# Kernel optimization log

Measured on AMD Instinct MI355X. Metric: run time of the kernel, lower is better.

## Reference

```python
import jax, jax.numpy as jnp
import numpy as np
from functools import partial

B, N, K = 64, 1001, 10  # batch, n_nodes (incl. depot), n_clusters


def setup_inputs() -> dict:
    key = jax.random.key(0)
    k1, k2, k3 = jax.random.split(key, 3)
    cluster_logits = jax.random.normal(k1, (B, N, K), dtype=jnp.float32)
    coords = jax.random.uniform(k2, (B, N, 2), dtype=jnp.float32)
    demands = jax.random.uniform(k3, (B, N), dtype=jnp.float32)
    capacity = jnp.ones((B,), dtype=jnp.float32) * 5.0
    return {"cluster_logits": cluster_logits, "coords": coords,
            "demands": demands, "capacity": capacity, "n_samples": 1}


def _routing_distance(depot, cust, dem, cap, assign, n_clusters):
    """Total NN-heuristic routing distance for one instance.
    depot: (2,), cust: (n,2), dem: (n,), cap: scalar, assign: (n,) int.
    """
    n = cust.shape[0]
    S = n_clusters * n  # max routes: route id = cluster * n + within-cluster route idx

    # --- greedy capacity split (sequential over customers in index order) ---
    def split_step(carry, x):
        loads, counts, nonempty = carry  # per-cluster state
        k, d = x
        start_new = (loads[k] + d > cap) & nonempty[k]
        new_count = counts[k] + start_new.astype(jnp.int32)
        new_load = jnp.where(start_new, d, loads[k] + d)
        carry = (loads.at[k].set(new_load), counts.at[k].set(new_count),
                 nonempty.at[k].set(True))
        return carry, new_count

    init = (jnp.zeros((n_clusters,), dem.dtype),
            jnp.zeros((n_clusters,), jnp.int32),
            jnp.zeros((n_clusters,), bool))
    _, rid = jax.lax.scan(split_step, init, (assign.astype(jnp.int32), dem))
    seg = assign.astype(jnp.int32) * n + rid  # global route id per customer

    # --- nearest-neighbor routing, all routes advance one hop per scan step ---
    idx = jnp.arange(n)

    def nn_step(carry, _):
        visited, pos, acc = carry  # (n,), (S,2), (S,)
        cur = pos[seg]  # (n,2) current position of each customer's route
        d = jnp.sqrt(((cust - cur) ** 2).sum(-1))
        d = jnp.where(visited, jnp.inf, d)
        seg_min = jax.ops.segment_min(d, seg, num_segments=S)  # (S,)
        win = (~visited) & (d <= seg_min[seg])
        # lowest-index tie-break, matching the torch strict-< argmin
        win_idx = jax.ops.segment_min(jnp.where(win, idx, n), seg, num_segments=S)
        active = win_idx < n
        chosen = win & (idx == win_idx[seg])
        visited = visited | chosen
        acc = acc + jnp.where(active, seg_min, 0.0)
        new_pos = jnp.where(active[:, None], cust[jnp.clip(win_idx, 0, n - 1)], pos)
        return (visited, new_pos, acc), None

    pos0 = jnp.broadcast_to(depot, (S, 2))
    carry0 = (jnp.zeros((n,), bool), pos0, jnp.zeros((S,), cust.dtype))
    (visited, pos, acc), _ = jax.lax.scan(nn_step, carry0, None, length=n)

    # return-to-depot leg for every non-empty route
    route_used = jax.ops.segment_sum(jnp.ones((n,), cust.dtype), seg, num_segments=S) > 0
    acc = acc + jnp.where(route_used, jnp.sqrt(((pos - depot) ** 2).sum(-1)), 0.0)
    return acc.sum()


def _route_batch(coords, demands, capacity, assign, n_clusters):
    f = partial(_routing_distance, n_clusters=n_clusters)
    return jax.vmap(f)(coords[:, 0], coords[:, 1:], demands[:, 1:], capacity, assign)


def reference(cluster_logits, coords, demands, capacity, n_samples):
    batch_size, n_nodes, n_clusters = cluster_logits.shape
    customer_logits = cluster_logits[:, 1:, :]  # drop depot
    log_probs = jax.nn.log_softmax(customer_logits, axis=-1)

    key = jax.random.key(42)
    all_d, all_lp = [], []
    for s in range(n_samples):  # tiny fixed loop over samples
        ks = jax.random.fold_in(key, s)
        assignments = jax.random.categorical(ks, customer_logits, axis=-1)  # (B, n)
        slp = jnp.take_along_axis(log_probs, assignments[..., None], axis=-1)[..., 0]
        all_lp.append(slp.sum(-1))  # (B,)
        d = jax.lax.stop_gradient(
            _route_batch(coords, demands, capacity, assignments, n_clusters))
        all_d.append(d)

    distances = jnp.stack(all_d, axis=1)       # (B, n_samples)
    log_probs_stacked = jnp.stack(all_lp, axis=1)
    if n_samples > 1:
        baseline = jax.lax.stop_gradient(distances.mean(axis=1, keepdims=True))
    else:
        baseline = jax.lax.stop_gradient(distances.mean())
    advantage = distances - baseline
    reinforce_loss = (advantage * log_probs_stacked).sum() / (batch_size * n_samples)
    return reinforce_loss, distances.mean()
```

## Files before the change

### kernel.cpp

```cpp
#include <hip/hip_runtime.h>
#include <stdint.h>

#define BB 64
#define NC 1000
#define KC 10
#define MEMCAP 212
#define RCAP 64

__host__ __device__ inline void threefry2x32(uint32_t k0, uint32_t k1,
                                             uint32_t x0, uint32_t x1,
                                             uint32_t* o0, uint32_t* o1) {
  uint32_t k2 = k0 ^ k1 ^ 0x1BD11BDAu;
  x0 += k0; x1 += k1;
#define TF_R(R) { x0 += x1; x1 = (x1 << (R)) | (x1 >> (32 - (R))); x1 ^= x0; }
  TF_R(13) TF_R(15) TF_R(26) TF_R(6)
  x0 += k1; x1 += k2 + 1u;
  TF_R(17) TF_R(29) TF_R(16) TF_R(24)
  x0 += k2; x1 += k0 + 2u;
  TF_R(13) TF_R(15) TF_R(26) TF_R(6)
  x0 += k0; x1 += k1 + 3u;
  TF_R(17) TF_R(29) TF_R(16) TF_R(24)
  x0 += k1; x1 += k2 + 4u;
  TF_R(13) TF_R(15) TF_R(26) TF_R(6)
  x0 += k2; x1 += k0 + 5u;
#undef TF_R
  *o0 = x0; *o1 = x1;
}

__device__ inline uint32_t rand_bits(uint32_t ks0, uint32_t ks1, uint32_t p) {
  uint32_t a, b; threefry2x32(ks0, ks1, 0u, p, &a, &b); return b;
}

template <int CTRL>
__device__ __forceinline__ void dpp_min_step(unsigned long long& comb,
                                             float& x, float& y) {
  int lo = (int)(uint32_t)comb;
  int hi = (int)(uint32_t)(comb >> 32);
  int olo = __builtin_amdgcn_update_dpp(lo, lo, CTRL, 0xf, 0xf, false);
  int ohi = __builtin_amdgcn_update_dpp(hi, hi, CTRL, 0xf, 0xf, false);
  int oxi = __builtin_amdgcn_update_dpp(__float_as_int(x), __float_as_int(x),
                                        CTRL, 0xf, 0xf, false);
  int oyi = __builtin_amdgcn_update_dpp(__float_as_int(y), __float_as_int(y),
                                        CTRL, 0xf, 0xf, false);
  unsigned long long o =
      ((unsigned long long)(uint32_t)ohi << 32) | (uint32_t)olo;
  if (o < comb) { comb = o; x = __int_as_float(oxi); y = __int_as_float(oyi); }
}

template <int CTRL>
__device__ __forceinline__ void dpp_max_step(unsigned long long& pk, float& x) {
  int lo = (int)(uint32_t)pk;
  int hi = (int)(uint32_t)(pk >> 32);
  int olo = __builtin_amdgcn_update_dpp(lo, lo, CTRL, 0xf, 0xf, false);
  int ohi = __builtin_amdgcn_update_dpp(hi, hi, CTRL, 0xf, 0xf, false);
  int oxi = __builtin_amdgcn_update_dpp(__float_as_int(x), __float_as_int(x),
                                        CTRL, 0xf, 0xf, false);
  unsigned long long o =
      ((unsigned long long)(uint32_t)ohi << 32) | (uint32_t)olo;
  if (o > pk) { pk = o; x = __int_as_float(oxi); }
}

template <int CTRL>
__device__ __forceinline__ float dpp_fmax(float x) {
  int o = __builtin_amdgcn_update_dpp(__float_as_int(x), __float_as_int(x),
                                      CTRL, 0xf, 0xf, false);
  return fmaxf(x, __int_as_float(o));
}

template <int CTRL>
__device__ __forceinline__ float dpp_fadd(float x) {
  int o = __builtin_amdgcn_update_dpp(__float_as_int(x), __float_as_int(x),
                                      CTRL, 0xf, 0xf, false);
  return x + __int_as_float(o);
}

__global__ __launch_bounds__(256) void k_sample(
    const float* __restrict__ logits,
    uint32_t ks0, uint32_t ks1,
    uint8_t* __restrict__ assign,
    float* __restrict__ slp) {
  int gtid = blockIdx.x * 256 + threadIdx.x;
  int cust = gtid >> 4;
  int k = gtid & 15;
  int b = cust / NC, n = cust - b * NC;
  const float TINY = 1.1754943508222875e-38f;
  bool actk = (k < KC);

  float x = actk ? logits[((size_t)b * 1001 + (size_t)(n + 1)) * KC + k]
                 : -INFINITY;
  float v = -INFINITY;
  if (actk) {
    uint32_t bits = rand_bits(ks0, ks1, (uint32_t)cust * (uint32_t)KC + (uint32_t)k);
    float f = __uint_as_float((bits >> 9) | 0x3f800000u) - 1.0f;
    float u = (f > 0.0f) ? f : TINY;
    float g = -logf(-logf(u));
    v = g + x;
  }
  uint32_t uv = __float_as_uint(v);
  uint32_t key = (uv & 0x80000000u) ? ~uv : (uv | 0x80000000u);
  unsigned long long pk =
      ((unsigned long long)key << 32) | (uint32_t)(15 - k);
  float bwx = x;
  dpp_max_step<0xB1>(pk, bwx);
  dpp_max_step<0x4E>(pk, bwx);
  dpp_max_step<0x141>(pk, bwx);
  dpp_max_step<0x140>(pk, bwx);
  int best_k = 15 - (int)(pk & 0xFu);

  float xm = x;
  xm = dpp_fmax<0xB1>(xm); xm = dpp_fmax<0x4E>(xm);
  xm = dpp_fmax<0x141>(xm); xm = dpp_fmax<0x140>(xm);

  float es = actk ? expf(x - xm) : 0.0f;
  es = dpp_fadd<0xB1>(es); es = dpp_fadd<0x4E>(es);
  es = dpp_fadd<0x141>(es); es = dpp_fadd<0x140>(es);

  if (k == 0) {
    slp[cust] = (bwx - xm) - logf(es);
    assign[cust] = (uint8_t)best_k;
  }
}

__global__ __launch_bounds__(128, 1) void k_route(
    const float* __restrict__ coords,
    const float* __restrict__ demands,
    const float* __restrict__ capacity,
    const uint8_t* __restrict__ assign,
    const float* __restrict__ slp,
    double* __restrict__ pdistc,
    double* __restrict__ lp) {
  int b = blockIdx.x / 6;
  int blk = blockIdx.x % 6;
  int tid = threadIdx.x;
  int w = tid >> 6, lane = tid & 63;

  __shared__ float memx[2][MEMCAP], memy[2][MEMCAP], demp[2][MEMCAP];
  __shared__ uint16_t rsw[2][RCAP], rlw[2][RCAP];

  if (blk == 5) {
    if (w == 0) {
      const float4* s4 = reinterpret_cast<const float4*>(slp + (size_t)b * NC);
      double acc = 0.0;
#pragma unroll
      for (int t = 0; t < 4; ++t) {
        int idx = t * 64 + lane;
        if (idx < 250) {
          float4 v = s4[idx];
          acc += (double)v.x + (double)v.y + (double)v.z + (double)v.w;
        }
      }
#pragma unroll
      for (int m = 1; m < 64; m <<= 1) acc += __shfl_xor(acc, m);
      if (lane == 0) lp[b] = acc;
    }
    return;
  }

  int myk = blk * 2 + w;
  const float* cb = coords + (size_t)b * 1001 * 2;
  const float2* cb2 = reinterpret_cast<const float2*>(cb);
  const float* db = demands + (size_t)b * 1001;
  const uint8_t* ab = assign + (size_t)b * NC;
  float cap = capacity[b];
  float dx0 = cb[0], dy0 = cb[1];

#pragma unroll
  for (int t = 0; t < 4; ++t) {
    int i = t * 64 + lane;
    if (i < MEMCAP) demp[w][i] = 0.0f;
  }

  int ci0 = lane * 16;
  float X[16], Y[16], D[16];
  uint32_t A[16];
#pragma unroll
  for (int j = 0; j < 16; ++j) { X[j] = 0.0f; Y[j] = 0.0f; D[j] = 0.0f; A[j] = 0xFFu; }

  if (lane < 62) {
    const uint4* ap = reinterpret_cast<const uint4*>(ab + ci0);
    const float4* cp = reinterpret_cast<const float4*>(cb + 2 * ci0);
    const float4* dp = reinterpret_cast<const float4*>(db + ci0);
    uint4 a4 = ap[0];
    float4 c0 = cp[0], c1 = cp[1], c2 = cp[2], c3 = cp[3], c4 = cp[4],
           c5 = cp[5], c6 = cp[6], c7 = cp[7], c8 = cp[8];
    float4 e0 = dp[0], e1 = dp[1], e2 = dp[2], e3 = dp[3], e4 = dp[4];
    A[0]  =  a4.x        & 0xFFu; A[1]  = (a4.x >>  8) & 0xFFu;
    A[2]  = (a4.x >> 16) & 0xFFu; A[3]  = (a4.x >> 24) & 0xFFu;
    A[4]  =  a4.y        & 0xFFu; A[5]  = (a4.y >>  8) & 0xFFu;
    A[6]  = (a4.y >> 16) & 0xFFu; A[7]  = (a4.y >> 24) & 0xFFu;
    A[8]  =  a4.z        & 0xFFu; A[9]  = (a4.z >>  8) & 0xFFu;
    A[10] = (a4.z >> 16) & 0xFFu; A[11] = (a4.z >> 24) & 0xFFu;
    A[12] =  a4.w        & 0xFFu; A[13] = (a4.w >>  8) & 0xFFu;
    A[14] = (a4.w >> 16) & 0xFFu; A[15] = (a4.w >> 24) & 0xFFu;
    X[0]  = c0.z; Y[0]  = c0.w;  X[1]  = c1.x; Y[1]  = c1.y;
    X[2]  = c1.z; Y[2]  = c1.w;  X[3]  = c2.x; Y[3]  = c2.y;
    X[4]  = c2.z; Y[4]  = c2.w;  X[5]  = c3.x; Y[5]  = c3.y;
    X[6]  = c3.z; Y[6]  = c3.w;  X[7]  = c4.x; Y[7]  = c4.y;
    X[8]  = c4.z; Y[8]  = c4.w;  X[9]  = c5.x; Y[9]  = c5.y;
    X[10] = c5.z; Y[10] = c5.w;  X[11] = c6.x; Y[11] = c6.y;
    X[12] = c6.z; Y[12] = c6.w;  X[13] = c7.x; Y[13] = c7.y;
    X[14] = c7.z; Y[14] = c7.w;  X[15] = c8.x; Y[15] = c8.y;
    D[0]  = e0.y; D[1]  = e0.z; D[2]  = e0.w; D[3]  = e1.x;
    D[4]  = e1.y; D[5]  = e1.z; D[6]  = e1.w; D[7]  = e2.x;
    D[8]  = e2.y; D[9]  = e2.z; D[10] = e2.w; D[11] = e3.x;
    D[12] = e3.y; D[13] = e3.z; D[14] = e3.w; D[15] = e4.x;
  } else if (lane == 62) {
#pragma unroll
    for (int j = 0; j < 8; ++j) {
      int ci = 992 + j;
      A[j] = ab[ci];
      float2 c = cb2[ci + 1];
      X[j] = c.x; Y[j] = c.y;
      D[j] = db[ci + 1];
    }
  }

  int cnt = 0;
#pragma unroll
  for (int j = 0; j < 16; ++j) cnt += (A[j] == (uint32_t)myk);
  int xs = cnt;
#pragma unroll
  for (int off = 1; off < 64; off <<= 1) {
    int v = __shfl_up(xs, off);
    if (lane >= off) xs += v;
  }
  int pos = xs - cnt;
  int mcount = __shfl(xs, 63);

#pragma unroll
  for (int j = 0; j < 16; ++j) {
    if (A[j] == (uint32_t)myk && pos < MEMCAP) {
      memx[w][pos] = X[j];
      memy[w][pos] = Y[j];
      demp[w][pos] = D[j];
      pos++;
    }
  }
  int M = (mcount < MEMCAP) ? mcount : MEMCAP;

  int rcount = 0;
  if (lane == 0 && M > 0) {
    const float4* dp4 = reinterpret_cast<const float4*>(&demp[w][0]);
    float load = 0.0f;
    int cur = 0, r = 0;
    int trips = (M + 3) >> 2;
    float4 cv = dp4[0];
    float4 nv = dp4[1];
    for (int t = 0; t < trips; ++t) {
      float4 nv2 = dp4[t + 2];
#define SPLIT_E(DV, E)                                                        \
      {                                                                       \
        int j = t * 4 + E;                                                    \
        float d = DV;                                                         \
        if (j == 0) load = d;                                                 \
        else if (load + d > cap) {                                            \
          rsw[w][r] = (uint16_t)cur; rlw[w][r] = (uint16_t)(j - cur);         \
          r++; cur = j; load = d;                                             \
        } else load += d;                \
      }
      SPLIT_E(cv.x, 0) SPLIT_E(cv.y, 1) SPLIT_E(cv.z, 2) SPLIT_E(cv.w, 3)
#undef SPLIT_E
      cv = nv; nv = nv2;
    }
    rsw[w][r] = (uint16_t)cur;
    rlw[w][r] = (uint16_t)(M - cur);
    r++;
    rcount = r;
  }
  rcount = __shfl(rcount, 0);

  int lane16 = lane & 15;
  int grp = lane >> 4;
  double gacc = 0.0;

  for (int r = grp; r < rcount; r += 4) {
    int start = rsw[w][r];
    int L = rlw[w][r];
    float px = dx0, py = dy0, racc = 0.0f;

    if (L <= 16) {
      float mx = 0.0f, my = 0.0f;
      bool act = (lane16 < L);
      if (act) { mx = memx[w][start + lane16]; my = memy[w][start + lane16]; }
      uint32_t unv = act ? 1u : 0u;
      for (int step = 0; step < L; ++step) {
        float bd = INFINITY, bx = 0.0f, by = 0.0f;
        if (unv) {
          float ddx = mx - px, ddy = my - py;
          bd = sqrtf(ddx * ddx + ddy * ddy);
          bx = mx; by = my;
        }
        unsigned long long comb = unv
            ? ((((unsigned long long)__float_as_uint(bd)) << 32) |
               (unsigned)lane16)
            : ~0ull;
        dpp_min_step<0xB1>(comb, bx, by);
        dpp_min_step<0x4E>(comb, bx, by);
        dpp_min_step<0x141>(comb, bx, by);
        dpp_min_step<0x140>(comb, bx, by);
        int wl = (int)(comb & 0xFFFFFFFFull);
        float best = __uint_as_float((uint32_t)(comb >> 32));
        if (wl == (int)lane16) unv = 0;
        px = bx; py = by;
        racc += best;
      }
    } else {
      float mx0 = 0, my0 = 0, mx1 = 0, my1 = 0, mx2 = 0, my2 = 0, mx3 = 0, my3 = 0;
      uint32_t vis = 0;
#define LOADC(c, MX, MY)                                                      \
      { int s = (c) * 16 + lane16;                                            \
        if (s < L) { MX = memx[w][start + s]; MY = memy[w][start + s]; }      \
        else vis |= (1u << (c)); }
      LOADC(0, mx0, my0) LOADC(1, mx1, my1) LOADC(2, mx2, my2) LOADC(3, mx3, my3)
#undef LOADC
      for (int step = 0; step < L; ++step) {
        float bd = INFINITY; int bc = -1; float bx = 0, by = 0;
#define CAND(c, MX, MY)                                                       \
        if (!(vis & (1u << (c)))) {                                           \
          float ddx = MX - px, ddy = MY - py;                                 \
          float d = sqrtf(ddx * ddx + ddy * ddy);                             \
          if (d < bd) { bd = d; bc = (c); bx = MX; by = MY; }                 \
        }
        CAND(0, mx0, my0) CAND(1, mx1, my1) CAND(2, mx2, my2) CAND(3, mx3, my3)
#undef CAND
        unsigned long long comb = (bc < 0)
            ? ~0ull
            : (((unsigned long long)__float_as_uint(bd)) << 32) |
              (unsigned)(bc * 16 + lane16);
        dpp_min_step<0xB1>(comb, bx, by);
        dpp_min_step<0x4E>(comb, bx, by);
        dpp_min_step<0x141>(comb, bx, by);
        dpp_min_step<0x140>(comb, bx, by);
        int slot = (int)(comb & 0xFFFFFFFFull);
        float best = __uint_as_float((uint32_t)(comb >> 32));
        int src16 = slot & 15, cu = slot >> 4;
        if (src16 == (int)lane16) vis |= (1u << cu);
        px = bx; py = by;
        racc += best;
      }
    }
    float ddx = px - dx0, ddy = py - dy0;
    racc += sqrtf(ddx * ddx + ddy * ddy);
    gacc += (double)racc;
  }

  {
    double t2 = (lane16 == 0) ? gacc : 0.0;
#pragma unroll
    for (int m = 1; m < 64; m <<= 1) t2 += __shfl_xor(t2, m);
    if (lane == 0) pdistc[b * KC + myk] = t2;
  }
}

__global__ __launch_bounds__(64) void k_final(
    const double* __restrict__ pdistc,
    const double* __restrict__ lp,
    float* __restrict__ out) {
  int tid = threadIdx.x;
  double dd = 0.0;
#pragma unroll
  for (int k = 0; k < KC; ++k) dd += pdistc[tid * KC + k];
  float df = (float)dd;
  float lf = (float)lp[tid];
  double m = (double)df;
#pragma unroll
  for (int m2 = 1; m2 < 64; m2 <<= 1) m += __shfl_xor(m, m2);
  double mean = m / 64.0;
  float meanf = (float)mean;
  double li = ((double)df - (double)meanf) * (double)lf;
#pragma unroll
  for (int m2 = 1; m2 < 64; m2 <<= 1) li += __shfl_xor(li, m2);
  if (tid == 0) {
    out[0] = (float)(li / 64.0);
    out[1] = meanf;
  }
}

extern "C" void kernel_launch(void* const* d_in, const int* in_sizes, int n_in,
                              void* d_out, int out_size, void* d_ws, size_t ws_size,
                              hipStream_t stream) {
  const float* logits   = (const float*)d_in[0];
  const float* coords   = (const float*)d_in[1];
  const float* demands  = (const float*)d_in[2];
  const float* capacity = (const float*)d_in[3];

  uint8_t* ws = (uint8_t*)d_ws;
  double*  pdistc = (double*)(ws);
  double*  lp     = (double*)(ws + 8192);
  uint8_t* assign = (uint8_t*)(ws + 9216);
  float*   slp    = (float*)(ws + 73216);

  uint32_t ks0, ks1;
  threefry2x32(0u, 42u, 0u, 0u, &ks0, &ks1);

  k_sample<<<dim3(BB * NC * 16 / 256), dim3(256), 0, stream>>>(
      logits, ks0, ks1, assign, slp);
  k_route<<<dim3(BB * 6), dim3(128), 0, stream>>>(
      coords, demands, capacity, assign, slp, pdistc, lp);
  k_final<<<dim3(1), dim3(64), 0, stream>>>(pdistc, lp, (float*)d_out);
}
```

Baseline: 34.15 us.

## Consolidate per-batch routing into one 704-thread block covering all clusters

Replaces the six 128-thread blocks per batch instance with a single 704-thread block: ten waves each handle one cluster and an eleventh wave sums the log-probabilities. Shared buffers grow to hold all ten clusters. This cuts the block count and launch granularity and keeps each batch's coordinates local to one CU. In exchange, far fewer CUs are occupied and several waves share each SIMD, which can serialize the latency-bound nearest-neighbour loops.

```diff
diff --git a/kernel.cpp b/kernel.cpp
--- a/kernel.cpp
+++ b/kernel.cpp
@@ -121,7 +121,7 @@
   }
 }
 
-__global__ __launch_bounds__(128, 1) void k_route(
+__global__ __launch_bounds__(704, 1) void k_route(
     const float* __restrict__ coords,
     const float* __restrict__ demands,
     const float* __restrict__ capacity,
@@ -129,34 +129,31 @@
     const float* __restrict__ slp,
     double* __restrict__ pdistc,
     double* __restrict__ lp) {
-  int b = blockIdx.x / 6;
-  int blk = blockIdx.x % 6;
+  int b = blockIdx.x;
   int tid = threadIdx.x;
   int w = tid >> 6, lane = tid & 63;
 
-  __shared__ float memx[2][MEMCAP], memy[2][MEMCAP], demp[2][MEMCAP];
-  __shared__ uint16_t rsw[2][RCAP], rlw[2][RCAP];
-
-  if (blk == 5) {
-    if (w == 0) {
-      const float4* s4 = reinterpret_cast<const float4*>(slp + (size_t)b * NC);
-      double acc = 0.0;
-#pragma unroll
-      for (int t = 0; t < 4; ++t) {
-        int idx = t * 64 + lane;
-        if (idx < 250) {
-          float4 v = s4[idx];
-          acc += (double)v.x + (double)v.y + (double)v.z + (double)v.w;
-        }
+  __shared__ float memx[KC][MEMCAP], memy[KC][MEMCAP], demp[KC][MEMCAP];
+  __shared__ uint16_t rsw[KC][RCAP], rlw[KC][RCAP];
+
+  if (w == 10) {
+    const float4* s4 = reinterpret_cast<const float4*>(slp + (size_t)b * NC);
+    double acc = 0.0;
+#pragma unroll
+    for (int t = 0; t < 4; ++t) {
+      int idx = t * 64 + lane;
+      if (idx < 250) {
+        float4 v = s4[idx];
+        acc += (double)v.x + (double)v.y + (double)v.z + (double)v.w;
       }
-#pragma unroll
-      for (int m = 1; m < 64; m <<= 1) acc += __shfl_xor(acc, m);
-      if (lane == 0) lp[b] = acc;
-    }
+    }
+#pragma unroll
+    for (int m = 1; m < 64; m <<= 1) acc += __shfl_xor(acc, m);
+    if (lane == 0) lp[b] = acc;
     return;
   }
 
-  int myk = blk * 2 + w;
+  int myk = w;
   const float* cb = coords + (size_t)b * 1001 * 2;
   const float2* cb2 = reinterpret_cast<const float2*>(cb);
   const float* db = demands + (size_t)b * 1001;
@@ -167,7 +164,7 @@
 #pragma unroll
   for (int t = 0; t < 4; ++t) {
     int i = t * 64 + lane;
-    if (i < MEMCAP) demp[w][i] = 0.0f;
+    if (i < MEMCAP) demp[myk][i] = 0.0f;
   }
 
   int ci0 = lane * 16;
@@ -230,9 +227,9 @@
 #pragma unroll
   for (int j = 0; j < 16; ++j) {
     if (A[j] == (uint32_t)myk && pos < MEMCAP) {
-      memx[w][pos] = X[j];
-      memy[w][pos] = Y[j];
-      demp[w][pos] = D[j];
+      memx[myk][pos] = X[j];
+      memy[myk][pos] = Y[j];
+      demp[myk][pos] = D[j];
       pos++;
     }
   }
@@ -240,7 +237,7 @@
 
   int rcount = 0;
   if (lane == 0 && M > 0) {
-    const float4* dp4 = reinterpret_cast<const float4*>(&demp[w][0]);
+    const float4* dp4 = reinterpret_cast<const float4*>(&demp[myk][0]);
     float load = 0.0f;
     int cur = 0, r = 0;
     int trips = (M + 3) >> 2;
@@ -254,7 +251,7 @@
         float d = DV;                                                         \
         if (j == 0) load = d;                                                 \
         else if (load + d > cap) {                                            \
-          rsw[w][r] = (uint16_t)cur; rlw[w][r] = (uint16_t)(j - cur);         \
+          rsw[myk][r] = (uint16_t)cur; rlw[myk][r] = (uint16_t)(j - cur);     \
           r++; cur = j; load = d;                                             \
         } else load += d;                \
       }
@@ -262,8 +259,8 @@
 #undef SPLIT_E
       cv = nv; nv = nv2;
     }
-    rsw[w][r] = (uint16_t)cur;
-    rlw[w][r] = (uint16_t)(M - cur);
+    rsw[myk][r] = (uint16_t)cur;
+    rlw[myk][r] = (uint16_t)(M - cur);
     r++;
     rcount = r;
   }
@@ -274,14 +271,14 @@
   double gacc = 0.0;
 
   for (int r = grp; r < rcount; r += 4) {
-    int start = rsw[w][r];
-    int L = rlw[w][r];
+    int start = rsw[myk][r];
+    int L = rlw[myk][r];
     float px = dx0, py = dy0, racc = 0.0f;
 
     if (L <= 16) {
       float mx = 0.0f, my = 0.0f;
       bool act = (lane16 < L);
-      if (act) { mx = memx[w][start + lane16]; my = memy[w][start + lane16]; }
+      if (act) { mx = memx[myk][start + lane16]; my = memy[myk][start + lane16]; }
       uint32_t unv = act ? 1u : 0u;
       for (int step = 0; step < L; ++step) {
         float bd = INFINITY, bx = 0.0f, by = 0.0f;
@@ -309,7 +306,7 @@
       uint32_t vis = 0;
 #define LOADC(c, MX, MY)                                                      \
       { int s = (c) * 16 + lane16;                                            \
-        if (s < L) { MX = memx[w][start + s]; MY = memy[w][start + s]; }      \
+        if (s < L) { MX = memx[myk][start + s]; MY = memy[myk][start + s]; }  \
         else vis |= (1u << (c)); }
       LOADC(0, mx0, my0) LOADC(1, mx1, my1) LOADC(2, mx2, my2) LOADC(3, mx3, my3)
 #undef LOADC
@@ -395,7 +392,7 @@
 
   k_sample<<<dim3(BB * NC * 16 / 256), dim3(256), 0, stream>>>(
       logits, ks0, ks1, assign, slp);
-  k_route<<<dim3(BB * 6), dim3(128), 0, stream>>>(
+  k_route<<<dim3(BB), dim3(704), 0, stream>>>(
       coords, demands, capacity, assign, slp, pdistc, lp);
   k_final<<<dim3(1), dim3(64), 0, stream>>>(pdistc, lp, (float*)d_out);
 }
```

After: 39.34 us. 1.15x slower.
